# Performance work log

Hardware: AMD Instinct MI355X
Metric: run time of the kernel (lower is better)

## Reference

```python
import jax, jax.numpy as jnp
import numpy as np
import math

B, N, K, S = 4, 128, 250, 250   # batch, channels(d_model), chunk len, num chunks
M = 64 // 2                      # d_state complex modes (conjugate-pair S4D param.)


def setup_inputs() -> dict:
    key = jax.random.key(0)
    ks = jax.random.split(key, 24)
    d = {"x": jax.random.normal(ks[0], (B, N, K, S), jnp.float32)}
    i = 1
    for p in ("intra", "inter"):
        # S4D (diagonal SSM) parameters
        d[p + "_log_dt"] = (jax.random.uniform(ks[i], (N,), jnp.float32)
                            * (math.log(0.1) - math.log(0.001)) + math.log(0.001))
        d[p + "_logA_re"] = jnp.full((N, M), math.log(0.5), jnp.float32)
        d[p + "_A_im"] = jnp.tile(math.pi * jnp.arange(M, dtype=jnp.float32), (N, 1))
        d[p + "_C_re"] = jax.random.normal(ks[i + 1], (N, M), jnp.float32) * (0.5 ** 0.5)
        d[p + "_C_im"] = jax.random.normal(ks[i + 2], (N, M), jnp.float32) * (0.5 ** 0.5)
        d[p + "_D"] = jax.random.normal(ks[i + 3], (N,), jnp.float32)
        # S4 output position-wise linear (H -> 2H) + GLU
        d[p + "_ow"] = jax.random.normal(ks[i + 4], (2 * N, N), jnp.float32) / math.sqrt(N)
        d[p + "_ob"] = jnp.zeros((2 * N,), jnp.float32)
        # block linear
        d[p + "_lw"] = jax.random.normal(ks[i + 5], (N, N), jnp.float32) / math.sqrt(N)
        d[p + "_lb"] = jnp.zeros((N,), jnp.float32)
        # GroupNorm(1, N)
        d[p + "_gg"] = jnp.ones((N,), jnp.float32)
        d[p + "_gb"] = jnp.zeros((N,), jnp.float32)
        i += 6
    return d


def _s4(u, log_dt, logA_re, A_im, C_re, C_im, D, ow, ob):
    # u: [b, H, L] (transposed layout). S4D kernel + FFT conv + GELU + GLU out.
    L = u.shape[-1]
    dt = jnp.exp(log_dt)                              # [H]
    A = -jnp.exp(logA_re) + 1j * A_im                 # [H, M]
    dtA = dt[:, None] * A                             # [H, M]
    C = (C_re + 1j * C_im) * (jnp.exp(dtA) - 1.0) / A # ZOH-discretized C
    vand = jnp.exp(dtA[:, :, None] * jnp.arange(L, dtype=jnp.float32))  # [H, M, L]
    kern = 2.0 * jnp.einsum('hm,hml->hl', C, vand).real                 # [H, L]
    n = 2 * L
    y = jnp.fft.irfft(jnp.fft.rfft(u, n) * jnp.fft.rfft(kern, n), n)[..., :L]
    y = y + D[:, None] * u
    y = jax.nn.gelu(y)
    y = jnp.einsum('oh,bhl->bol', ow, y) + ob[None, :, None]            # [b, 2H, L]
    y1, y2 = jnp.split(y, 2, axis=1)
    return y1 * jax.nn.sigmoid(y2)                                      # GLU -> [b, H, L]


def _group_norm(x, g, b, eps=1e-8):
    mu = jnp.mean(x, axis=(1, 2, 3), keepdims=True)
    var = jnp.var(x, axis=(1, 2, 3), keepdims=True)
    return (x - mu) / jnp.sqrt(var + eps) * g[None, :, None, None] + b[None, :, None, None]


def reference(x,
              intra_log_dt, intra_logA_re, intra_A_im, intra_C_re, intra_C_im,
              intra_D, intra_ow, intra_ob, intra_lw, intra_lb, intra_gg, intra_gb,
              inter_log_dt, inter_logA_re, inter_A_im, inter_C_re, inter_C_im,
              inter_D, inter_ow, inter_ob, inter_lw, inter_lb, inter_gg, inter_gb):
    Bx, Nx, Kx, Sx = x.shape
    # intra (within-chunk) path: sequence length = K
    intra = jnp.transpose(x, (0, 3, 1, 2)).reshape(Bx * Sx, Nx, Kx)
    intra = _s4(intra, intra_log_dt, intra_logA_re, intra_A_im,
                intra_C_re, intra_C_im, intra_D, intra_ow, intra_ob)
    # faithful to torch: .view(B*S*K, -1) on contiguous [B*S, N, K]
    intra = (intra.reshape(Bx * Sx * Kx, -1) @ intra_lw.T + intra_lb).reshape(Bx * Sx, Nx, Kx)
    intra = jnp.transpose(intra.reshape(Bx, Sx, Nx, Kx), (0, 2, 3, 1))  # [B,N,K,S]
    intra = _group_norm(intra, intra_gg, intra_gb) + x
    # inter (across-chunk) path: sequence length = S
    inter = jnp.transpose(intra, (0, 2, 1, 3)).reshape(Bx * Kx, Nx, Sx)
    inter = _s4(inter, inter_log_dt, inter_logA_re, inter_A_im,
                inter_C_re, inter_C_im, inter_D, inter_ow, inter_ob)
    inter = (inter.reshape(Bx * Kx * Sx, -1) @ inter_lw.T + inter_lb).reshape(Bx * Kx, Nx, Sx)
    inter = jnp.transpose(inter.reshape(Bx, Kx, Nx, Sx), (0, 2, 1, 3))  # [B,N,K,S]
    inter = _group_norm(inter, inter_gg, inter_gb)
    return inter + intra
```

## Files before the change

kernel.cpp:

```cpp
#include <hip/hip_runtime.h>
#include <math.h>

#define NTOT 32000000

typedef __attribute__((ext_vector_type(8))) short bf8_t;
typedef __attribute__((ext_vector_type(4))) float f4_t;

__device__ __forceinline__ float fast_tanh(float t) {
    return 1.0f - 2.0f / (1.0f + __expf(2.0f * t));
}
__device__ __forceinline__ float gelu_f(float v) {
    return 0.5f * v * (1.0f + fast_tanh(0.7978845608028654f * (v + 0.044715f * v * v * v)));
}
__device__ __forceinline__ float sigmoid_f(float v) {
    return 1.0f / (1.0f + __expf(-v));
}
__device__ __forceinline__ unsigned short f2bf(float f) {
    unsigned u = __float_as_uint(f);
    u = (u + 0x7FFFu + ((u >> 16) & 1u)) >> 16;
    return (unsigned short)u;
}
__device__ __forceinline__ float bf2f(unsigned short u) {
    return __uint_as_float(((unsigned)u) << 16);
}
__device__ __forceinline__ unsigned swz(unsigned a) {
    return a ^ (((a >> 9) & 7u) << 4);
}
__device__ __forceinline__ unsigned fxor(int row) {
    return ((unsigned)(row & 1) << 6) ^ ((unsigned)((row >> 1) & 7) << 4);
}

__global__ void wc_kernel(const float* __restrict__ log_dt, const float* __restrict__ logA_re,
                          const float* __restrict__ A_im, const float* __restrict__ C_re,
                          const float* __restrict__ C_im, float* __restrict__ wC) {
    int t = blockIdx.x * 256 + threadIdx.x;
    if (t >= 128 * 32) return;
    int h = t >> 5, m = t & 31;
    float dt  = expf(log_dt[h]);
    float are = -expf(logA_re[t]);
    float aim = A_im[t];
    float er  = expf(dt * are);
    float wr  = er * cosf(dt * aim);
    float wi  = er * sinf(dt * aim);
    float e1r = wr - 1.0f, e1i = wi;
    float inv = 1.0f / (are * are + aim * aim);
    float qr  = (e1r * are + e1i * aim) * inv;
    float qi  = (e1i * are - e1r * aim) * inv;
    float cre = C_re[t], cim = C_im[t];
    wC[h * 128 + m]      = dt * are;
    wC[h * 128 + 32 + m] = dt * aim;
    wC[h * 128 + 64 + m] = 2.0f * (cre * qr - cim * qi);
    wC[h * 128 + 96 + m] = 2.0f * (cre * qi + cim * qr);
}

__global__ void kern_kernel(const float* __restrict__ wC, const float* __restrict__ Dv,
                            float* __restrict__ kern) {
    int h = blockIdx.x, l = threadIdx.x;
    const float* wc = wC + (h << 7);
    float acc = 0.0f;
    if (l < 250) {
        float fl = (float)l;
#pragma unroll 1
        for (int m = 0; m < 32; ++m) {
            float er  = expf(wc[m] * fl);
            float ang = wc[32 + m] * fl;
            float sv, cv;
            sincosf(ang, &sv, &cv);
            acc += er * (wc[64 + m] * cv - wc[96 + m] * sv);
        }
        if (l == 0) acc += Dv[h];
    }
    kern[(h << 8) + l] = acc;
}

__global__ void frag_kernel(const float* __restrict__ kern, unsigned short* __restrict__ fragH,
                            unsigned short* __restrict__ fragL) {
    int h = blockIdx.x, d16 = blockIdx.y, lane = threadIdx.x;
    int lid = lane & 15, q = lane >> 4;
    const float* kh = kern + (h << 8);
    bf8_t vh, vl;
#pragma unroll
    for (int j = 0; j < 8; ++j) {
        int idx = d16 * 16 + lid - 8 * q - j;
        float v = (idx >= 0) ? kh[idx] : 0.0f;
        unsigned short hb = f2bf(v);
        vh[j] = (short)hb;
        vl[j] = (short)f2bf(v - bf2f(hb));
    }
    long off = ((long)((h << 4) + d16) * 64 + lane) * 8;
    *(bf8_t*)(fragH + off) = vh;
    *(bf8_t*)(fragL + off) = vl;
}

__global__ void cvtw_kernel(const float* __restrict__ ow, const float* __restrict__ lw,
                            unsigned short* __restrict__ owbf, unsigned short* __restrict__ lwbf) {
    int t = blockIdx.x * 256 + threadIdx.x;
    if (t < 32768) owbf[t] = f2bf(ow[t]);
    else if (t < 49152) lwbf[t - 32768] = f2bf(lw[t - 32768]);
}

__global__ __launch_bounds__(256, 3)
void conv_kernel(const float* __restrict__ in, unsigned short* __restrict__ Y,
                 const unsigned short* __restrict__ fragH, const unsigned short* __restrict__ fragL,
                 int inter) {
    __shared__ unsigned short Bhi[64 * 256];
    __shared__ unsigned short Blo[64 * 64];
    const int tid = threadIdx.x;
    const int lane = tid & 63, wave = tid >> 6;
    const int lid = lane & 15, quad = lane >> 4;
    const int a = wave >> 1, p = wave & 1;
    const int s0 = blockIdx.x * 64;
    const int h = blockIdx.y, b = blockIdx.z;
    const float* src = in + (long)(b * 128 + h) * 62500;
    char* BhiB = (char*)Bhi;
    char* BloB = (char*)Blo;
    const int q8 = tid >> 5;
    const int spL = (tid & 31) << 1;

    f4_t acc[4][4];
#pragma unroll
    for (int rt = 0; rt < 4; ++rt)
#pragma unroll
        for (int ct = 0; ct < 4; ++ct) acc[rt][ct] = (f4_t)0.0f;

    float2 pf[4];
    auto loadc = [&](int c) {
        if (!inter) {
#pragma unroll
            for (int it = 0; it < 4; ++it) {
                int k = (c << 5) + q8 * 4 + it;
                bool v = (k < 250) && (s0 + spL < 250);
                pf[it] = v ? *(const float2*)(src + (long)k * 250 + s0 + spL)
                           : make_float2(0.0f, 0.0f);
            }
        } else {
#pragma unroll
            for (int it = 0; it < 4; ++it) {
                int i = tid + it * 256;
                int sq = i >> 4;
                int tt = (i & 15) << 1;
                int t = (c << 5) + tt;
                bool v = (s0 + sq < 250) && (t < 250);
                pf[it] = v ? *(const float2*)(src + (long)(s0 + sq) * 250 + t)
                           : make_float2(0.0f, 0.0f);
            }
        }
    };
    auto storec = [&](int c) {
        if (!inter) {
            unsigned wx0 = 0, wx1 = 0, wy0 = 0, wy1 = 0;
            unsigned lx0 = 0, lx1 = 0, ly0 = 0, ly1 = 0;
#pragma unroll
            for (int it = 0; it < 4; ++it) {
                unsigned short hx = f2bf(pf[it].x), hy = f2bf(pf[it].y);
                unsigned short lx = f2bf(pf[it].x - bf2f(hx));
                unsigned short ly = f2bf(pf[it].y - bf2f(hy));
                if (it < 2) {
                    wx0 |= (unsigned)hx << (16 * it); wy0 |= (unsigned)hy << (16 * it);
                    lx0 |= (unsigned)lx << (16 * it); ly0 |= (unsigned)ly << (16 * it);
                } else {
                    wx1 |= (unsigned)hx << (16 * (it - 2)); wy1 |= (unsigned)hy << (16 * (it - 2));
                    lx1 |= (unsigned)lx << (16 * (it - 2)); ly1 |= (unsigned)ly << (16 * (it - 2));
                }
            }
            unsigned colB = (unsigned)((c << 6) + (q8 << 3));
            unsigned a0 = ((unsigned)(spL * 512) + colB) ^ fxor(spL);
            unsigned a1 = ((unsigned)((spL + 1) * 512) + colB) ^ fxor(spL + 1);
            *(uint2*)(BhiB + a0) = make_uint2(wx0, wx1);
            *(uint2*)(BhiB + a1) = make_uint2(wy0, wy1);
            unsigned c0 = ((unsigned)(spL * 128) + (unsigned)(q8 << 3)) ^ fxor(spL);
            unsigned c1 = ((unsigned)((spL + 1) * 128) + (unsigned)(q8 << 3)) ^ fxor(spL + 1);
            *(uint2*)(BloB + c0) = make_uint2(lx0, lx1);
            *(uint2*)(BloB + c1) = make_uint2(ly0, ly1);
        } else {
#pragma unroll
            for (int it = 0; it < 4; ++it) {
                int i = tid + it * 256;
                int sq = i >> 4;
                int tt = (i & 15) << 1;
                unsigned short hx = f2bf(pf[it].x);
                unsigned short hy = f2bf(pf[it].y);
                unsigned b0 = ((unsigned)(sq * 512 + ((c << 5) + tt) * 2)) ^ fxor(sq);
                *(unsigned*)(BhiB + b0) = (unsigned)hx | ((unsigned)hy << 16);
                unsigned short lx = f2bf(pf[it].x - bf2f(hx));
                unsigned short ly = f2bf(pf[it].y - bf2f(hy));
                unsigned b1 = ((unsigned)(sq * 128 + tt * 2)) ^ fxor(sq);
                *(unsigned*)(BloB + b1) = (unsigned)lx | ((unsigned)ly << 16);
            }
        }
    };

    loadc(0);
#pragma unroll 1
    for (int c = 0; c < 8; ++c) {
        __syncthreads();
        storec(c);
        __syncthreads();
        if (c < 7) loadc(c + 1);
        bf8_t bh[4], bl[4];
#pragma unroll
        for (int ct = 0; ct < 4; ++ct) {
            int row = ct * 16 + lid;
            bh[ct] = *(const bf8_t*)(BhiB + (((unsigned)(row * 512 + c * 64 + quad * 16)) ^ fxor(row)));
            bl[ct] = *(const bf8_t*)(BloB + (((unsigned)(row * 128 + quad * 16)) ^ fxor(row)));
        }
#pragma unroll
        for (int rt = 0; rt < 4; ++rt) {
            int n = 2 * rt + a - c;
            if (n >= 0) {
                long fo = ((long)((h << 4) + 2 * n + p) * 64 + lane) * 8;
                bf8_t fh = *(const bf8_t*)(fragH + fo);
                bf8_t fl = *(const bf8_t*)(fragL + fo);
#pragma unroll
                for (int ct = 0; ct < 4; ++ct) {
                    acc[rt][ct] = __builtin_amdgcn_mfma_f32_16x16x32_bf16(fh, bh[ct], acc[rt][ct], 0, 0, 0);
                    acc[rt][ct] = __builtin_amdgcn_mfma_f32_16x16x32_bf16(fh, bl[ct], acc[rt][ct], 0, 0, 0);
                    acc[rt][ct] = __builtin_amdgcn_mfma_f32_16x16x32_bf16(fl, bh[ct], acc[rt][ct], 0, 0, 0);
                }
            }
        }
    }
    __syncthreads();
#pragma unroll
    for (int rt = 0; rt < 4; ++rt) {
        const int l0 = rt * 64 + wave * 16 + quad * 4;
#pragma unroll
        for (int ct = 0; ct < 4; ++ct) {
            const int sq = ct * 16 + lid;
            unsigned lo = (unsigned)f2bf(gelu_f(acc[rt][ct][0])) |
                          ((unsigned)f2bf(gelu_f(acc[rt][ct][1])) << 16);
            unsigned hi = (unsigned)f2bf(gelu_f(acc[rt][ct][2])) |
                          ((unsigned)f2bf(gelu_f(acc[rt][ct][3])) << 16);
            unsigned byteO = ((unsigned)(sq * 512 + l0 * 2)) ^ fxor(sq);
            *(uint2*)(BhiB + byteO) = make_uint2(lo, hi);
        }
    }
    __syncthreads();
    unsigned int* Yg = (unsigned int*)Y + ((long)(b * 250 + s0) * 128 + h) * 125;
#pragma unroll 1
    for (int i = tid; i < 8192; i += 256) {
        int sq = i >> 7, e = i & 127;
        if (e < 125 && s0 + sq < 250) {
            unsigned v = *(unsigned*)(BhiB + (((unsigned)(sq * 512 + e * 4)) ^ fxor(sq)));
            Yg[(long)sq * 16000 + e] = v;
        }
    }
}

__global__ __launch_bounds__(256, 3)
void mlp_kernel(const unsigned short* __restrict__ Ybf, const unsigned short* __restrict__ owbf,
                const float* __restrict__ ob, const unsigned short* __restrict__ lwbf,
                const float* __restrict__ lb, float* __restrict__ V, float* __restrict__ part) {
    __shared__ unsigned short ZL[16000];
    __shared__ unsigned short Yt[32 * 128];
    const int tid = threadIdx.x;
    const int lane = tid & 63, wave = tid >> 6;
    const int lid = lane & 15, quad = lane >> 4;
    const int seq = blockIdx.x, hf = blockIdx.y;
    const unsigned short* Ys = Ybf + (long)seq * 32000;
    char* YtB = (char*)Yt;
    char* ZLB = (char*)ZL;

    const int tA = 4 * hf + wave;
    const int tB = 8 + 4 * hf + wave;
    bf8_t wf[4][2];
#pragma unroll
    for (int c = 0; c < 4; ++c) {
        wf[c][0] = *(const bf8_t*)(owbf + (tA * 16 + lid) * 128 + c * 32 + quad * 8);
        wf[c][1] = *(const bf8_t*)(owbf + (tB * 16 + lid) * 128 + c * 32 + quad * 8);
    }
    float ob1[4], ob2[4];
#pragma unroll
    for (int reg = 0; reg < 4; ++reg) {
        int hp = wave * 16 + quad * 4 + reg;
        ob1[reg] = ob[64 * hf + hp];
        ob2[reg] = ob[128 + 64 * hf + hp];
    }

    unsigned int pf[8];
    auto loadc = [&](int l0) {
#pragma unroll
        for (int it = 0; it < 8; ++it) {
            int i = tid + it * 256;
            int hh = i >> 4;
            int l = l0 + (i & 15) * 2;
            pf[it] = (l < 250) ? *(const unsigned int*)(Ys + hh * 250 + l) : 0u;
        }
    };
    auto storec = [&]() {
#pragma unroll
        for (int it = 0; it < 8; ++it) {
            int i = tid + it * 256;
            int hh = i >> 4;
            int l2 = (i & 15) * 2;
            unsigned a0 = ((unsigned)(l2 * 256 + hh * 2)) ^ fxor(l2);
            unsigned a1 = ((unsigned)((l2 + 1) * 256 + hh * 2)) ^ fxor(l2 + 1);
            *(unsigned short*)(YtB + a0) = (unsigned short)(pf[it] & 0xFFFF);
            *(unsigned short*)(YtB + a1) = (unsigned short)(pf[it] >> 16);
        }
    };

    loadc(0);
#pragma unroll 1
    for (int ch = 0; ch < 8; ++ch) {
        __syncthreads();
        storec();
        __syncthreads();
        if (ch < 7) loadc((ch + 1) * 32);
        f4_t acc[2][2];
#pragma unroll
        for (int pp = 0; pp < 2; ++pp)
#pragma unroll
            for (int jj = 0; jj < 2; ++jj) acc[pp][jj] = (f4_t)0.0f;
#pragma unroll
        for (int c = 0; c < 4; ++c) {
            bf8_t bfr[2];
#pragma unroll
            for (int jj = 0; jj < 2; ++jj) {
                int row = jj * 16 + lid;
                bfr[jj] = *(const bf8_t*)(YtB + (((unsigned)(row * 256 + c * 64 + quad * 16)) ^ fxor(row)));
            }
#pragma unroll
            for (int pp = 0; pp < 2; ++pp)
#pragma unroll
                for (int jj = 0; jj < 2; ++jj)
                    acc[pp][jj] = __builtin_amdgcn_mfma_f32_16x16x32_bf16(wf[c][pp], bfr[jj], acc[pp][jj], 0, 0, 0);
        }
        const int lbase = ch * 32;
#pragma unroll
        for (int reg = 0; reg < 4; ++reg) {
            int hp = wave * 16 + quad * 4 + reg;
#pragma unroll
            for (int jj = 0; jj < 2; ++jj) {
                int l = lbase + jj * 16 + lid;
                if (l < 250) {
                    float z1 = acc[0][jj][reg] + ob1[reg];
                    float z2 = acc[1][jj][reg] + ob2[reg];
                    unsigned aB = swz((unsigned)(hp * 250 + l) * 2u);
                    *(unsigned short*)(ZLB + aB) = f2bf(z1 * sigmoid_f(z2));
                }
            }
        }
    }
    __syncthreads();

    f4_t acc2[2][8];
#pragma unroll
    for (int mt = 0; mt < 2; ++mt)
#pragma unroll
        for (int nt = 0; nt < 8; ++nt) acc2[mt][nt] = (f4_t)0.0f;
    const int jl0 = wave * 32;
#pragma unroll
    for (int c = 0; c < 4; ++c) {
        bf8_t af[2];
#pragma unroll
        for (int mt = 0; mt < 2; ++mt) {
            int jl = jl0 + mt * 16 + lid;
            if (jl > 124) jl = 124;
            af[mt] = *(const bf8_t*)(ZLB + swz((unsigned)(jl * 128 + c * 32 + quad * 8) * 2u));
        }
#pragma unroll
        for (int nt = 0; nt < 8; ++nt) {
            bf8_t bfr = *(const bf8_t*)(lwbf + (nt * 16 + lid) * 128 + c * 32 + quad * 8);
#pragma unroll
            for (int mt = 0; mt < 2; ++mt)
                acc2[mt][nt] = __builtin_amdgcn_mfma_f32_16x16x32_bf16(af[mt], bfr, acc2[mt][nt], 0, 0, 0);
        }
    }
    float s = 0.0f, q = 0.0f;
    float* Vs = V + (long)seq * 32000 + hf * 16000;
#pragma unroll
    for (int nt = 0; nt < 8; ++nt) {
        int o = nt * 16 + lid;
        float bb = lb[o];
#pragma unroll
        for (int mt = 0; mt < 2; ++mt)
#pragma unroll
            for (int reg = 0; reg < 4; ++reg) {
                int jlr = jl0 + mt * 16 + quad * 4 + reg;
                if (jlr < 125) {
                    float v = acc2[mt][nt][reg] + bb;
                    Vs[jlr * 128 + o] = v;
                    s += v;
                    q += v * v;
                }
            }
    }
    __syncthreads();
    float* red = (float*)Yt;
    red[tid] = s;
    red[256 + tid] = q;
    __syncthreads();
    for (int st = 128; st > 0; st >>= 1) {
        if (tid < st) {
            red[tid] += red[tid + st];
            red[256 + tid] += red[256 + tid + st];
        }
        __syncthreads();
    }
    if (tid == 0) {
        part[(seq * 2 + hf) * 2]     = red[0];
        part[(seq * 2 + hf) * 2 + 1] = red[256];
    }
}

__global__ void stats_final_kernel(const float* __restrict__ part, float* __restrict__ stats) {
    __shared__ double ssum[256], ssq[256];
    const int b = blockIdx.x;
    double s = 0.0, q = 0.0;
    for (int i = threadIdx.x; i < 500; i += 256) {
        s += (double)part[(b * 500 + i) * 2];
        q += (double)part[(b * 500 + i) * 2 + 1];
    }
    ssum[threadIdx.x] = s; ssq[threadIdx.x] = q;
    __syncthreads();
    for (int st = 128; st > 0; st >>= 1) {
        if (threadIdx.x < st) {
            ssum[threadIdx.x] += ssum[threadIdx.x + st];
            ssq[threadIdx.x]  += ssq[threadIdx.x + st];
        }
        __syncthreads();
    }
    if (threadIdx.x == 0) {
        double mu = ssum[0] / 8000000.0;
        double var = ssq[0] / 8000000.0 - mu * mu;
        stats[b * 2] = (float)mu;
        stats[b * 2 + 1] = (float)(1.0 / sqrt(var + 1e-8));
    }
}

__global__ void intra_fin_kernel(const float* __restrict__ f, const float* __restrict__ x,
                                 const float* __restrict__ stats, const float* __restrict__ gg,
                                 const float* __restrict__ gb, float* __restrict__ out) {
    __shared__ float tile[32][33];
    int kt = blockIdx.x, st = blockIdx.y;
    int bn = blockIdx.z; int b = bn >> 7, n = bn & 127;
    int tx = threadIdx.x & 31, ty = threadIdx.x >> 5;
    const float mu = stats[b * 2], rs = stats[b * 2 + 1];
    const float ga = gg[n] * rs, bb = gb[n];
    const float* fb = f + (long)(b * 250) * 32000 + n * 250;
#pragma unroll
    for (int j = 0; j < 4; ++j) {
        int k = kt * 32 + tx;
        int s = st * 32 + ty + j * 8;
        if (k < 250 && s < 250) tile[ty + j * 8][tx] = fb[(long)s * 32000 + k];
    }
    __syncthreads();
#pragma unroll
    for (int j = 0; j < 4; ++j) {
        int s = st * 32 + tx;
        int k = kt * 32 + ty + j * 8;
        if (k < 250 && s < 250) {
            long idx = ((long)(b * 128 + n) * 250 + k) * 250 + s;
            out[idx] = (tile[tx][ty + j * 8] - mu) * ga + bb + x[idx];
        }
    }
}

__global__ void final_kernel(const float* __restrict__ f2, const float* __restrict__ stats,
                             const float* __restrict__ gg, const float* __restrict__ gb,
                             float* __restrict__ out) {
    long g = (long)blockIdx.x * 256 + threadIdx.x;
    if (g >= NTOT) return;
    int s = (int)(g % 250); long r = g / 250;
    int k = (int)(r % 250); long bn = r / 250;
    int n = (int)(bn % 128); int b = (int)(bn / 128);
    float mu = stats[b * 2], rs = stats[b * 2 + 1];
    float v = f2[((long)(b * 250 + k) * 128 + n) * 250 + s];
    out[g] = (v - mu) * rs * gg[n] + gb[n] + out[g];
}

extern "C" void kernel_launch(void* const* d_in, const int* in_sizes, int n_in,
                              void* d_out, int out_size, void* d_ws, size_t ws_size,
                              hipStream_t stream) {
    (void)in_sizes; (void)n_in; (void)out_size; (void)ws_size;
    const float* x = (const float*)d_in[0];
    float* out = (float*)d_out;
    char* base = (char*)d_ws;
    float* V            = (float*)base;
    unsigned short* Ybf = (unsigned short*)(base + 128000000L);
    float* wC           = (float*)(base + 256000000L);
    unsigned short* owbf= (unsigned short*)(base + 256065536L);
    unsigned short* lwbf= (unsigned short*)(base + 256131072L);
    float* part         = (float*)(base + 256163840L);
    float* stats        = (float*)(base + 256180224L);
    float* kern         = (float*)(base + 118000000L);
    unsigned short* fragH = (unsigned short*)(base + 120000000L);
    unsigned short* fragL = (unsigned short*)(base + 123000000L);

    const float* i_logdt = (const float*)d_in[1];
    const float* i_logA  = (const float*)d_in[2];
    const float* i_Aim   = (const float*)d_in[3];
    const float* i_Cre   = (const float*)d_in[4];
    const float* i_Cim   = (const float*)d_in[5];
    const float* i_D     = (const float*)d_in[6];
    const float* i_ow    = (const float*)d_in[7];
    const float* i_ob    = (const float*)d_in[8];
    const float* i_lw    = (const float*)d_in[9];
    const float* i_lb    = (const float*)d_in[10];
    const float* i_gg    = (const float*)d_in[11];
    const float* i_gb    = (const float*)d_in[12];
    const float* e_logdt = (const float*)d_in[13];
    const float* e_logA  = (const float*)d_in[14];
    const float* e_Aim   = (const float*)d_in[15];
    const float* e_Cre   = (const float*)d_in[16];
    const float* e_Cim   = (const float*)d_in[17];
    const float* e_D     = (const float*)d_in[18];
    const float* e_ow    = (const float*)d_in[19];
    const float* e_ob    = (const float*)d_in[20];
    const float* e_lw    = (const float*)d_in[21];
    const float* e_lb    = (const float*)d_in[22];
    const float* e_gg    = (const float*)d_in[23];
    const float* e_gb    = (const float*)d_in[24];

    wc_kernel<<<16, 256, 0, stream>>>(i_logdt, i_logA, i_Aim, i_Cre, i_Cim, wC);
    kern_kernel<<<128, 256, 0, stream>>>(wC, i_D, kern);
    frag_kernel<<<dim3(128, 16), 64, 0, stream>>>(kern, fragH, fragL);
    cvtw_kernel<<<192, 256, 0, stream>>>(i_ow, i_lw, owbf, lwbf);
    conv_kernel<<<dim3(4, 128, 4), 256, 0, stream>>>(x, Ybf, fragH, fragL, 0);
    mlp_kernel<<<dim3(1000, 2), 256, 0, stream>>>(Ybf, owbf, i_ob, lwbf, i_lb, V, part);
    stats_final_kernel<<<4, 256, 0, stream>>>(part, stats);
    intra_fin_kernel<<<dim3(8, 8, 512), 256, 0, stream>>>(V, x, stats, i_gg, i_gb, out);

    wc_kernel<<<16, 256, 0, stream>>>(e_logdt, e_logA, e_Aim, e_Cre, e_Cim, wC);
    kern_kernel<<<128, 256, 0, stream>>>(wC, e_D, kern);
    frag_kernel<<<dim3(128, 16), 64, 0, stream>>>(kern, fragH, fragL);
    cvtw_kernel<<<192, 256, 0, stream>>>(e_ow, e_lw, owbf, lwbf);
    conv_kernel<<<dim3(4, 128, 4), 256, 0, stream>>>(out, Ybf, fragH, fragL, 1);
    mlp_kernel<<<dim3(1000, 2), 256, 0, stream>>>(Ybf, owbf, e_ob, lwbf, e_lb, V, part);
    stats_final_kernel<<<4, 256, 0, stream>>>(part, stats);
    final_kernel<<<NTOT / 256, 256, 0, stream>>>(V, stats, e_gg, e_gb, out);
}
```

Baseline: 839.7 us.

## Stage full hi/lo input tile in LDS once and use packed bf16 converts

The conv kernel now loads and splits the whole 256-column input tile into bf16 hi and lo parts in shared memory up front, instead of streaming 32-column chunks with two barriers per chunk. The lo buffer grows to full size and occupancy is lowered from 3 to 2 blocks per CU. Scalar bf16 rounding is replaced by the hardware v_cvt_pk_bf16_f32 instruction, both for the split and for the GELU output. This removes per-chunk synchronisation and conversion ALU work, at the cost of more LDS per block, lower occupancy and no overlap between loads and MFMA.

```diff
diff --git a/kernel.cpp b/kernel.cpp
--- a/kernel.cpp
+++ b/kernel.cpp
@@ -22,6 +22,11 @@
 }
 __device__ __forceinline__ float bf2f(unsigned short u) {
     return __uint_as_float(((unsigned)u) << 16);
+}
+__device__ __forceinline__ unsigned cvtpk(float a, float b) {
+    unsigned r;
+    asm("v_cvt_pk_bf16_f32 %0, %1, %2" : "=v"(r) : "v"(a), "v"(b));
+    return r;
 }
 __device__ __forceinline__ unsigned swz(unsigned a) {
     return a ^ (((a >> 9) & 7u) << 4);
@@ -99,12 +104,12 @@
     else if (t < 49152) lwbf[t - 32768] = f2bf(lw[t - 32768]);
 }
 
-__global__ __launch_bounds__(256, 3)
+__global__ __launch_bounds__(256, 2)
 void conv_kernel(const float* __restrict__ in, unsigned short* __restrict__ Y,
                  const unsigned short* __restrict__ fragH, const unsigned short* __restrict__ fragL,
                  int inter) {
     __shared__ unsigned short Bhi[64 * 256];
-    __shared__ unsigned short Blo[64 * 64];
+    __shared__ unsigned short Blo[64 * 256];
     const int tid = threadIdx.x;
     const int lane = tid & 63, wave = tid >> 6;
     const int lid = lane & 15, quad = lane >> 4;
@@ -117,15 +122,10 @@
     const int q8 = tid >> 5;
     const int spL = (tid & 31) << 1;
 
-    f4_t acc[4][4];
-#pragma unroll
-    for (int rt = 0; rt < 4; ++rt)
-#pragma unroll
-        for (int ct = 0; ct < 4; ++ct) acc[rt][ct] = (f4_t)0.0f;
-
-    float2 pf[4];
-    auto loadc = [&](int c) {
-        if (!inter) {
+    if (!inter) {
+#pragma unroll
+        for (int c = 0; c < 8; ++c) {
+            float2 pf[4];
 #pragma unroll
             for (int it = 0; it < 4; ++it) {
                 int k = (c << 5) + q8 * 4 + it;
@@ -133,7 +133,29 @@
                 pf[it] = v ? *(const float2*)(src + (long)k * 250 + s0 + spL)
                            : make_float2(0.0f, 0.0f);
             }
-        } else {
+            unsigned hx0 = cvtpk(pf[0].x, pf[1].x);
+            unsigned hx1 = cvtpk(pf[2].x, pf[3].x);
+            unsigned hy0 = cvtpk(pf[0].y, pf[1].y);
+            unsigned hy1 = cvtpk(pf[2].y, pf[3].y);
+            unsigned lx0 = cvtpk(pf[0].x - __uint_as_float(hx0 << 16),
+                                 pf[1].x - __uint_as_float(hx0 & 0xFFFF0000u));
+            unsigned lx1 = cvtpk(pf[2].x - __uint_as_float(hx1 << 16),
+                                 pf[3].x - __uint_as_float(hx1 & 0xFFFF0000u));
+            unsigned ly0 = cvtpk(pf[0].y - __uint_as_float(hy0 << 16),
+                                 pf[1].y - __uint_as_float(hy0 & 0xFFFF0000u));
+            unsigned ly1 = cvtpk(pf[2].y - __uint_as_float(hy1 << 16),
+                                 pf[3].y - __uint_as_float(hy1 & 0xFFFF0000u));
+            unsigned colB = (unsigned)((c << 6) + (q8 << 3));
+            unsigned a0 = ((unsigned)(spL * 512) + colB) ^ fxor(spL);
+            unsigned a1 = ((unsigned)((spL + 1) * 512) + colB) ^ fxor(spL + 1);
+            *(uint2*)(BhiB + a0) = make_uint2(hx0, hx1);
+            *(uint2*)(BhiB + a1) = make_uint2(hy0, hy1);
+            *(uint2*)(BloB + a0) = make_uint2(lx0, lx1);
+            *(uint2*)(BloB + a1) = make_uint2(ly0, ly1);
+        }
+    } else {
+#pragma unroll
+        for (int c = 0; c < 8; ++c) {
 #pragma unroll
             for (int it = 0; it < 4; ++it) {
                 int i = tid + it * 256;
@@ -141,68 +163,33 @@
                 int tt = (i & 15) << 1;
                 int t = (c << 5) + tt;
                 bool v = (s0 + sq < 250) && (t < 250);
-                pf[it] = v ? *(const float2*)(src + (long)(s0 + sq) * 250 + t)
-                           : make_float2(0.0f, 0.0f);
+                float2 pf = v ? *(const float2*)(src + (long)(s0 + sq) * 250 + t)
+                              : make_float2(0.0f, 0.0f);
+                unsigned hp = cvtpk(pf.x, pf.y);
+                unsigned lp = cvtpk(pf.x - __uint_as_float(hp << 16),
+                                    pf.y - __uint_as_float(hp & 0xFFFF0000u));
+                unsigned b0 = ((unsigned)(sq * 512 + t * 2)) ^ fxor(sq);
+                *(unsigned*)(BhiB + b0) = hp;
+                *(unsigned*)(BloB + b0) = lp;
             }
         }
-    };
-    auto storec = [&](int c) {
-        if (!inter) {
-            unsigned wx0 = 0, wx1 = 0, wy0 = 0, wy1 = 0;
-            unsigned lx0 = 0, lx1 = 0, ly0 = 0, ly1 = 0;
-#pragma unroll
-            for (int it = 0; it < 4; ++it) {
-                unsigned short hx = f2bf(pf[it].x), hy = f2bf(pf[it].y);
-                unsigned short lx = f2bf(pf[it].x - bf2f(hx));
-                unsigned short ly = f2bf(pf[it].y - bf2f(hy));
-                if (it < 2) {
-                    wx0 |= (unsigned)hx << (16 * it); wy0 |= (unsigned)hy << (16 * it);
-                    lx0 |= (unsigned)lx << (16 * it); ly0 |= (unsigned)ly << (16 * it);
-                } else {
-                    wx1 |= (unsigned)hx << (16 * (it - 2)); wy1 |= (unsigned)hy << (16 * (it - 2));
-                    lx1 |= (unsigned)lx << (16 * (it - 2)); ly1 |= (unsigned)ly << (16 * (it - 2));
-                }
-            }
-            unsigned colB = (unsigned)((c << 6) + (q8 << 3));
-            unsigned a0 = ((unsigned)(spL * 512) + colB) ^ fxor(spL);
-            unsigned a1 = ((unsigned)((spL + 1) * 512) + colB) ^ fxor(spL + 1);
-            *(uint2*)(BhiB + a0) = make_uint2(wx0, wx1);
-            *(uint2*)(BhiB + a1) = make_uint2(wy0, wy1);
-            unsigned c0 = ((unsigned)(spL * 128) + (unsigned)(q8 << 3)) ^ fxor(spL);
-            unsigned c1 = ((unsigned)((spL + 1) * 128) + (unsigned)(q8 << 3)) ^ fxor(spL + 1);
-            *(uint2*)(BloB + c0) = make_uint2(lx0, lx1);
-            *(uint2*)(BloB + c1) = make_uint2(ly0, ly1);
-        } else {
-#pragma unroll
-            for (int it = 0; it < 4; ++it) {
-                int i = tid + it * 256;
-                int sq = i >> 4;
-                int tt = (i & 15) << 1;
-                unsigned short hx = f2bf(pf[it].x);
-                unsigned short hy = f2bf(pf[it].y);
-                unsigned b0 = ((unsigned)(sq * 512 + ((c << 5) + tt) * 2)) ^ fxor(sq);
-                *(unsigned*)(BhiB + b0) = (unsigned)hx | ((unsigned)hy << 16);
-                unsigned short lx = f2bf(pf[it].x - bf2f(hx));
-                unsigned short ly = f2bf(pf[it].y - bf2f(hy));
-                unsigned b1 = ((unsigned)(sq * 128 + tt * 2)) ^ fxor(sq);
-                *(unsigned*)(BloB + b1) = (unsigned)lx | ((unsigned)ly << 16);
-            }
-        }
-    };
-
-    loadc(0);
-#pragma unroll 1
+    }
+    __syncthreads();
+
+    f4_t acc[4][4];
+#pragma unroll
+    for (int rt = 0; rt < 4; ++rt)
+#pragma unroll
+        for (int ct = 0; ct < 4; ++ct) acc[rt][ct] = (f4_t)0.0f;
+#pragma unroll 2
     for (int c = 0; c < 8; ++c) {
-        __syncthreads();
-        storec(c);
-        __syncthreads();
-        if (c < 7) loadc(c + 1);
         bf8_t bh[4], bl[4];
 #pragma unroll
         for (int ct = 0; ct < 4; ++ct) {
             int row = ct * 16 + lid;
-            bh[ct] = *(const bf8_t*)(BhiB + (((unsigned)(row * 512 + c * 64 + quad * 16)) ^ fxor(row)));
-            bl[ct] = *(const bf8_t*)(BloB + (((unsigned)(row * 128 + quad * 16)) ^ fxor(row)));
+            unsigned byteB = (((unsigned)(row * 512 + c * 64 + quad * 16)) ^ fxor(row));
+            bh[ct] = *(const bf8_t*)(BhiB + byteB);
+            bl[ct] = *(const bf8_t*)(BloB + byteB);
         }
 #pragma unroll
         for (int rt = 0; rt < 4; ++rt) {
@@ -227,10 +214,8 @@
 #pragma unroll
         for (int ct = 0; ct < 4; ++ct) {
             const int sq = ct * 16 + lid;
-            unsigned lo = (unsigned)f2bf(gelu_f(acc[rt][ct][0])) |
-                          ((unsigned)f2bf(gelu_f(acc[rt][ct][1])) << 16);
-            unsigned hi = (unsigned)f2bf(gelu_f(acc[rt][ct][2])) |
-                          ((unsigned)f2bf(gelu_f(acc[rt][ct][3])) << 16);
+            unsigned lo = cvtpk(gelu_f(acc[rt][ct][0]), gelu_f(acc[rt][ct][1]));
+            unsigned hi = cvtpk(gelu_f(acc[rt][ct][2]), gelu_f(acc[rt][ct][3]));
             unsigned byteO = ((unsigned)(sq * 512 + l0 * 2)) ^ fxor(sq);
             *(uint2*)(BhiB + byteO) = make_uint2(lo, hi);
         }
```

Measured after the change: 894.4 us. 1.07x slower.

## Split conv kernel across 8 waves with balanced triangular row pairing

Applied to the files above, without the earlier changes.

The Toeplitz-conv kernel moves from 4 to 8 waves per block. Each wave now owns two output row tiles (r and 15-r), so the causal triangular MFMA work is spread evenly across waves. The bf16 hi/lo split and the GELU output packing now use the packed v_cvt_pk_bf16_f32 instruction instead of manual rounding. The cost is more waves sharing the same LDS and a changed register budget through the new launch bounds.

```diff
diff --git a/kernel.cpp b/kernel.cpp
--- a/kernel.cpp
+++ b/kernel.cpp
@@ -22,6 +22,11 @@
 }
 __device__ __forceinline__ float bf2f(unsigned short u) {
     return __uint_as_float(((unsigned)u) << 16);
+}
+__device__ __forceinline__ unsigned cvtpk(float a, float b) {
+    unsigned r;
+    asm("v_cvt_pk_bf16_f32 %0, %1, %2" : "=v"(r) : "v"(a), "v"(b));
+    return r;
 }
 __device__ __forceinline__ unsigned swz(unsigned a) {
     return a ^ (((a >> 9) & 7u) << 4);
@@ -99,7 +104,7 @@
     else if (t < 49152) lwbf[t - 32768] = f2bf(lw[t - 32768]);
 }
 
-__global__ __launch_bounds__(256, 3)
+__global__ __launch_bounds__(512, 4)
 void conv_kernel(const float* __restrict__ in, unsigned short* __restrict__ Y,
                  const unsigned short* __restrict__ fragH, const unsigned short* __restrict__ fragL,
                  int inter) {
@@ -108,84 +113,72 @@
     const int tid = threadIdx.x;
     const int lane = tid & 63, wave = tid >> 6;
     const int lid = lane & 15, quad = lane >> 4;
-    const int a = wave >> 1, p = wave & 1;
     const int s0 = blockIdx.x * 64;
     const int h = blockIdx.y, b = blockIdx.z;
     const float* src = in + (long)(b * 128 + h) * 62500;
     char* BhiB = (char*)Bhi;
     char* BloB = (char*)Blo;
-    const int q8 = tid >> 5;
-    const int spL = (tid & 31) << 1;
-
-    f4_t acc[4][4];
-#pragma unroll
-    for (int rt = 0; rt < 4; ++rt)
-#pragma unroll
-        for (int ct = 0; ct < 4; ++ct) acc[rt][ct] = (f4_t)0.0f;
-
-    float2 pf[4];
+    const int r0 = wave;
+    const int r1 = 15 - wave;
+    const int kk2 = tid >> 5;
+    const int sp  = (tid & 31) << 1;
+
+    f4_t acc[2][4];
+#pragma unroll
+    for (int ri = 0; ri < 2; ++ri)
+#pragma unroll
+        for (int ct = 0; ct < 4; ++ct) acc[ri][ct] = (f4_t)0.0f;
+
+    float2 pv[2];
     auto loadc = [&](int c) {
         if (!inter) {
 #pragma unroll
-            for (int it = 0; it < 4; ++it) {
-                int k = (c << 5) + q8 * 4 + it;
-                bool v = (k < 250) && (s0 + spL < 250);
-                pf[it] = v ? *(const float2*)(src + (long)k * 250 + s0 + spL)
-                           : make_float2(0.0f, 0.0f);
+            for (int it = 0; it < 2; ++it) {
+                int k = (c << 5) + kk2 * 2 + it;
+                bool ok = (k < 250) && (s0 + sp < 250);
+                pv[it] = ok ? *(const float2*)(src + (long)k * 250 + s0 + sp)
+                            : make_float2(0.0f, 0.0f);
             }
         } else {
 #pragma unroll
-            for (int it = 0; it < 4; ++it) {
-                int i = tid + it * 256;
+            for (int it = 0; it < 2; ++it) {
+                int i = tid + (it << 9);
                 int sq = i >> 4;
                 int tt = (i & 15) << 1;
                 int t = (c << 5) + tt;
-                bool v = (s0 + sq < 250) && (t < 250);
-                pf[it] = v ? *(const float2*)(src + (long)(s0 + sq) * 250 + t)
-                           : make_float2(0.0f, 0.0f);
+                bool ok = (s0 + sq < 250) && (t < 250);
+                pv[it] = ok ? *(const float2*)(src + (long)(s0 + sq) * 250 + t)
+                            : make_float2(0.0f, 0.0f);
             }
         }
     };
     auto storec = [&](int c) {
         if (!inter) {
-            unsigned wx0 = 0, wx1 = 0, wy0 = 0, wy1 = 0;
-            unsigned lx0 = 0, lx1 = 0, ly0 = 0, ly1 = 0;
-#pragma unroll
-            for (int it = 0; it < 4; ++it) {
-                unsigned short hx = f2bf(pf[it].x), hy = f2bf(pf[it].y);
-                unsigned short lx = f2bf(pf[it].x - bf2f(hx));
-                unsigned short ly = f2bf(pf[it].y - bf2f(hy));
-                if (it < 2) {
-                    wx0 |= (unsigned)hx << (16 * it); wy0 |= (unsigned)hy << (16 * it);
-                    lx0 |= (unsigned)lx << (16 * it); ly0 |= (unsigned)ly << (16 * it);
-                } else {
-                    wx1 |= (unsigned)hx << (16 * (it - 2)); wy1 |= (unsigned)hy << (16 * (it - 2));
-                    lx1 |= (unsigned)lx << (16 * (it - 2)); ly1 |= (unsigned)ly << (16 * (it - 2));
-                }
-            }
-            unsigned colB = (unsigned)((c << 6) + (q8 << 3));
-            unsigned a0 = ((unsigned)(spL * 512) + colB) ^ fxor(spL);
-            unsigned a1 = ((unsigned)((spL + 1) * 512) + colB) ^ fxor(spL + 1);
-            *(uint2*)(BhiB + a0) = make_uint2(wx0, wx1);
-            *(uint2*)(BhiB + a1) = make_uint2(wy0, wy1);
-            unsigned c0 = ((unsigned)(spL * 128) + (unsigned)(q8 << 3)) ^ fxor(spL);
-            unsigned c1 = ((unsigned)((spL + 1) * 128) + (unsigned)(q8 << 3)) ^ fxor(spL + 1);
-            *(uint2*)(BloB + c0) = make_uint2(lx0, lx1);
-            *(uint2*)(BloB + c1) = make_uint2(ly0, ly1);
+            unsigned h0 = cvtpk(pv[0].x, pv[1].x);
+            unsigned h1 = cvtpk(pv[0].y, pv[1].y);
+            unsigned l0v = cvtpk(pv[0].x - __uint_as_float(h0 << 16),
+                                 pv[1].x - __uint_as_float(h0 & 0xFFFF0000u));
+            unsigned l1v = cvtpk(pv[0].y - __uint_as_float(h1 << 16),
+                                 pv[1].y - __uint_as_float(h1 & 0xFFFF0000u));
+            unsigned colH = (unsigned)((c << 6) + (kk2 << 2));
+            *(unsigned*)(BhiB + (((unsigned)(sp * 512) + colH) ^ fxor(sp)));
+            *(unsigned*)(BhiB + (((unsigned)(sp * 512) + colH) ^ fxor(sp))) = h0;
+            *(unsigned*)(BhiB + (((unsigned)((sp + 1) * 512) + colH) ^ fxor(sp + 1))) = h1;
+            unsigned colL = (unsigned)(kk2 << 2);
+            *(unsigned*)(BloB + (((unsigned)(sp * 128) + colL) ^ fxor(sp))) = l0v;
+            *(unsigned*)(BloB + (((unsigned)((sp + 1) * 128) + colL) ^ fxor(sp + 1))) = l1v;
         } else {
 #pragma unroll
-            for (int it = 0; it < 4; ++it) {
-                int i = tid + it * 256;
+            for (int it = 0; it < 2; ++it) {
+                int i = tid + (it << 9);
                 int sq = i >> 4;
                 int tt = (i & 15) << 1;
-                unsigned short hx = f2bf(pf[it].x);
-                unsigned short hy = f2bf(pf[it].y);
-                unsigned b0 = ((unsigned)(sq * 512 + ((c << 5) + tt) * 2)) ^ fxor(sq);
-                *(unsigned*)(BhiB + b0) = (unsigned)hx | ((unsigned)hy << 16);
-                unsigned short lx = f2bf(pf[it].x - bf2f(hx));
-                unsigned short ly = f2bf(pf[it].y - bf2f(hy));
-                unsigned b1 = ((unsigned)(sq * 128 + tt * 2)) ^ fxor(sq);
-                *(unsigned*)(BloB + b1) = (unsigned)lx | ((unsigned)ly << 16);
+                int t = (c << 5) + tt;
+                unsigned hp = cvtpk(pv[it].x, pv[it].y);
+                unsigned lp = cvtpk(pv[it].x - __uint_as_float(hp << 16),
+                                    pv[it].y - __uint_as_float(hp & 0xFFFF0000u));
+                *(unsigned*)(BhiB + (((unsigned)(sq * 512 + t * 2)) ^ fxor(sq))) = hp;
+                *(unsigned*)(BloB + (((unsigned)(sq * 128 + tt * 2)) ^ fxor(sq))) = lp;
             }
         }
     };
@@ -205,32 +198,31 @@
             bl[ct] = *(const bf8_t*)(BloB + (((unsigned)(row * 128 + quad * 16)) ^ fxor(row)));
         }
 #pragma unroll
-        for (int rt = 0; rt < 4; ++rt) {
-            int n = 2 * rt + a - c;
-            if (n >= 0) {
-                long fo = ((long)((h << 4) + 2 * n + p) * 64 + lane) * 8;
+        for (int ri = 0; ri < 2; ++ri) {
+            int r = ri ? r1 : r0;
+            if (r >= 2 * c) {
+                long fo = ((long)((h << 4) + (r - 2 * c)) * 64 + lane) * 8;
                 bf8_t fh = *(const bf8_t*)(fragH + fo);
                 bf8_t fl = *(const bf8_t*)(fragL + fo);
 #pragma unroll
                 for (int ct = 0; ct < 4; ++ct) {
-                    acc[rt][ct] = __builtin_amdgcn_mfma_f32_16x16x32_bf16(fh, bh[ct], acc[rt][ct], 0, 0, 0);
-                    acc[rt][ct] = __builtin_amdgcn_mfma_f32_16x16x32_bf16(fh, bl[ct], acc[rt][ct], 0, 0, 0);
-                    acc[rt][ct] = __builtin_amdgcn_mfma_f32_16x16x32_bf16(fl, bh[ct], acc[rt][ct], 0, 0, 0);
+                    acc[ri][ct] = __builtin_amdgcn_mfma_f32_16x16x32_bf16(fh, bh[ct], acc[ri][ct], 0, 0, 0);
+                    acc[ri][ct] = __builtin_amdgcn_mfma_f32_16x16x32_bf16(fh, bl[ct], acc[ri][ct], 0, 0, 0);
+                    acc[ri][ct] = __builtin_amdgcn_mfma_f32_16x16x32_bf16(fl, bh[ct], acc[ri][ct], 0, 0, 0);
                 }
             }
         }
     }
     __syncthreads();
 #pragma unroll
-    for (int rt = 0; rt < 4; ++rt) {
-        const int l0 = rt * 64 + wave * 16 + quad * 4;
+    for (int ri = 0; ri < 2; ++ri) {
+        const int r = ri ? r1 : r0;
+        const int l0 = r * 16 + quad * 4;
 #pragma unroll
         for (int ct = 0; ct < 4; ++ct) {
             const int sq = ct * 16 + lid;
-            unsigned lo = (unsigned)f2bf(gelu_f(acc[rt][ct][0])) |
-                          ((unsigned)f2bf(gelu_f(acc[rt][ct][1])) << 16);
-            unsigned hi = (unsigned)f2bf(gelu_f(acc[rt][ct][2])) |
-                          ((unsigned)f2bf(gelu_f(acc[rt][ct][3])) << 16);
+            unsigned lo = cvtpk(gelu_f(acc[ri][ct][0]), gelu_f(acc[ri][ct][1]));
+            unsigned hi = cvtpk(gelu_f(acc[ri][ct][2]), gelu_f(acc[ri][ct][3]));
             unsigned byteO = ((unsigned)(sq * 512 + l0 * 2)) ^ fxor(sq);
             *(uint2*)(BhiB + byteO) = make_uint2(lo, hi);
         }
@@ -238,7 +230,7 @@
     __syncthreads();
     unsigned int* Yg = (unsigned int*)Y + ((long)(b * 250 + s0) * 128 + h) * 125;
 #pragma unroll 1
-    for (int i = tid; i < 8192; i += 256) {
+    for (int i = tid; i < 8192; i += 512) {
         int sq = i >> 7, e = i & 127;
         if (e < 125 && s0 + sq < 250) {
             unsigned v = *(unsigned*)(BhiB + (((unsigned)(sq * 512 + e * 4)) ^ fxor(sq)));
@@ -517,7 +509,7 @@
     kern_kernel<<<128, 256, 0, stream>>>(wC, i_D, kern);
     frag_kernel<<<dim3(128, 16), 64, 0, stream>>>(kern, fragH, fragL);
     cvtw_kernel<<<192, 256, 0, stream>>>(i_ow, i_lw, owbf, lwbf);
-    conv_kernel<<<dim3(4, 128, 4), 256, 0, stream>>>(x, Ybf, fragH, fragL, 0);
+    conv_kernel<<<dim3(4, 128, 4), 512, 0, stream>>>(x, Ybf, fragH, fragL, 0);
     mlp_kernel<<<dim3(1000, 2), 256, 0, stream>>>(Ybf, owbf, i_ob, lwbf, i_lb, V, part);
     stats_final_kernel<<<4, 256, 0, stream>>>(part, stats);
     intra_fin_kernel<<<dim3(8, 8, 512), 256, 0, stream>>>(V, x, stats, i_gg, i_gb, out);
@@ -526,7 +518,7 @@
     kern_kernel<<<128, 256, 0, stream>>>(wC, e_D, kern);
     frag_kernel<<<dim3(128, 16), 64, 0, stream>>>(kern, fragH, fragL);
     cvtw_kernel<<<192, 256, 0, stream>>>(e_ow, e_lw, owbf, lwbf);
-    conv_kernel<<<dim3(4, 128, 4), 256, 0, stream>>>(out, Ybf, fragH, fragL, 1);
+    conv_kernel<<<dim3(4, 128, 4), 512, 0, stream>>>(out, Ybf, fragH, fragL, 1);
     mlp_kernel<<<dim3(1000, 2), 256, 0, stream>>>(Ybf, owbf, e_ob, lwbf, e_lb, V, part);
     stats_final_kernel<<<4, 256, 0, stream>>>(part, stats);
     final_kernel<<<NTOT / 256, 256, 0, stream>>>(V, stats, e_gg, e_gb, out);
```

Result: no change. 825.0 us (-1.8%).
